# Optimization experiments

Hardware: AMD Instinct MI355X
Metric: run time of the kernel (lower is better)

The kernel has to match this reference:

```python
import jax, jax.numpy as jnp
import numpy as np
jax.config.update("jax_enable_x64", True)

B, S, E, H, L, FF = 2, 1024, 768, 12, 4, 2048
MAX_THOUGHT_LEN = 3
LN_EPS = 1e-5

def _sinusoidal_pe(max_len, d):
    pos = np.arange(max_len)[:, None]
    div = np.exp(np.arange(0, d, 2) * (-np.log(10000.0) / d))
    pe = np.zeros((max_len, d), np.float32)
    pe[:, 0::2] = np.sin(pos * div)
    pe[:, 1::2] = np.cos(pos * div)
    return jnp.asarray(pe)

def _build_mask(Smax, thoughts_taken, n_tokens):
    # Vectorized equivalent of the torch loop building the block-causal mask.
    bs = thoughts_taken + 1
    i = np.arange(Smax)[:, None]
    j = np.arange(Smax)[None, :]
    same_block = (i // bs == j // bs) & (i // bs < n_tokens) & ((i % bs) >= (j % bs))
    start_vis = ((j % bs) == 0) & (j // bs < n_tokens) & (i > j) & (i < n_tokens * bs)
    allowed = same_block | start_vis
    # TransformerEncoder canonicalizes the bool mask: True (disallowed) -> -inf additive
    return jnp.asarray(np.where(allowed, 0.0, -np.inf).astype(np.float64))

def _layernorm(x, w, b):
    mu = jnp.mean(x, -1, keepdims=True)
    var = jnp.mean((x - mu) ** 2, -1, keepdims=True)
    return (x - mu) / jnp.sqrt(var + LN_EPS) * w + b

def setup_inputs() -> dict:
    key = jax.random.key(0)
    ks = jax.random.split(key, 8)
    f32 = jnp.float32
    return {
        "x": jax.random.normal(ks[0], (B, S, E), f32),
        "padding_mask": jnp.zeros((B, S), bool),
        "thought_pe": jax.random.normal(ks[1], (MAX_THOUGHT_LEN + 1, E), f32),
        "Wqkv": jax.random.normal(ks[2], (L, 3 * E, E), f32) * (E ** -0.5),
        "bqkv": jnp.zeros((L, 3 * E), f32),
        "W1": jax.random.normal(ks[3], (L, FF, E), f32) * (E ** -0.5),
        "b1": jnp.zeros((L, FF), f32),
        "W2": jax.random.normal(ks[4], (L, E, FF), f32) * (FF ** -0.5),
        "b2": jnp.zeros((L, E), f32),
        "ln1_w": jnp.ones((L, E), f32), "ln1_b": jnp.zeros((L, E), f32),
        "ln2_w": jnp.ones((L, E), f32), "ln2_b": jnp.zeros((L, E), f32),
        "lnf_w": jnp.ones((E,), f32), "lnf_b": jnp.zeros((E,), f32),
        "thoughts_taken": 1,
        "real_token_count": 512,
    }

def reference(x, padding_mask, thought_pe, Wqkv, bqkv, W1, b1, W2, b2,
              ln1_w, ln1_b, ln2_w, ln2_b, lnf_w, lnf_b,
              thoughts_taken, real_token_count):
    # NOTE: padding_mask is accepted but unused, matching the custom layer.
    nt = thoughts_taken + 1
    pe = _sinusoidal_pe(S, E)
    # DualPositionalEncoding (eval mode -> dropout is identity)
    h = x[:, : real_token_count * nt].reshape(B, real_token_count, nt, E)
    h = h + pe[:real_token_count][None, :, None, :] + thought_pe[:nt][None, None, :, :]
    h = h.reshape(B, real_token_count * nt, E)
    pad = S - real_token_count * nt
    if pad > 0:
        h = jnp.pad(h, ((0, 0), (0, pad), (0, 0)))
    mask = _build_mask(S, thoughts_taken, real_token_count)
    scale = 1.0 / jnp.sqrt(jnp.float64(E // H))
    for l in range(L):
        # manual fp64 attention, exactly as the torch layer
        s64 = h.astype(jnp.float64)
        qkv = s64 @ Wqkv[l].astype(jnp.float64).T + bqkv[l].astype(jnp.float64)
        q, k, v = jnp.split(qkv, 3, axis=-1)
        rh = lambda t: t.reshape(B, S, H, E // H).transpose(0, 2, 1, 3)
        q, k, v = rh(q), rh(k), rh(v)
        scores = jnp.einsum("bhqd,bhkd->bhqk", q, k) * scale + mask
        attn = jax.nn.softmax(scores, axis=-1)
        ao = jnp.einsum("bhqk,bhkd->bhqd", attn, v).transpose(0, 2, 1, 3).reshape(B, S, E)
        # NOTE: no out_proj -- the custom forward skips self_attn.out_proj
        h = _layernorm(h + ao.astype(h.dtype), ln1_w[l], ln1_b[l])
        ff = jax.nn.gelu(h @ W1[l].T + b1[l], approximate=False) @ W2[l].T + b2[l]
        h = _layernorm(h + ff, ln2_w[l], ln2_b[l])
        h = jnp.nan_to_num(h)
    return _layernorm(h, lnf_w, lnf_b)
```

## Files before the change

kernel.cpp:

```cpp
#include <hip/hip_runtime.h>
#include <math.h>

#define SEQ 1024
#define EMB 768
#define NHEAD 12
#define HDIM 64
#define NLAYER 4
#define FFDIM 2048
#define BATCH 2
#define ROWS (BATCH * SEQ)
#define BH (BATCH * NHEAD)
#define NCHUNK 2
#define CTILES 8

using f16 = _Float16;
using f16x4 = __attribute__((ext_vector_type(4))) _Float16;
using f16x8 = __attribute__((ext_vector_type(8))) _Float16;
using f32x4 = __attribute__((ext_vector_type(4))) float;
using f32x16 = __attribute__((ext_vector_type(16))) float;
typedef unsigned long long u64;

__device__ inline void gload16(const void* g, void* l) {
    __builtin_amdgcn_global_load_lds((const __attribute__((address_space(1))) unsigned*)g,
                                     (__attribute__((address_space(3))) unsigned*)l, 16, 0, 0);
}

__global__ void prep_kernel(const float* __restrict__ Wq, int na,
                            const float* __restrict__ W1, int nb,
                            const float* __restrict__ W2, int nc,
                            f16* __restrict__ oq, f16* __restrict__ o1, f16* __restrict__ o2,
                            const float* __restrict__ x,
                            const float* __restrict__ tpe,
                            float* __restrict__ h32,
                            f16* __restrict__ h16,
                            u64* __restrict__ mtab,
                            const int* __restrict__ tt_p,
                            const int* __restrict__ rtc_p) {
    const int ncast = na + nb + nc;
    const int nembed = BATCH * SEQ * EMB;
    const int nmask = SEQ * 16;
    const int total = ncast + nembed + nmask;
    const int nt = *tt_p + 1;
    const int rtc = *rtc_p;
    for (int i = blockIdx.x * blockDim.x + threadIdx.x; i < total;
         i += gridDim.x * blockDim.x) {
        if (i < ncast) {
            const float* src;
            f16* dst;
            int off;
            if (i < na)            { src = Wq; dst = oq; off = i; }
            else if (i < na + nb)  { src = W1; dst = o1; off = i - na; }
            else                   { src = W2; dst = o2; off = i - na - nb; }
            float4 v = ((const float4*)src)[off];
            f16x4 o;
            o[0] = (f16)v.x; o[1] = (f16)v.y; o[2] = (f16)v.z; o[3] = (f16)v.w;
            ((f16x4*)dst)[off] = o;
        } else if (i < ncast + nembed) {
            int idx = i - ncast;
            int e = idx % EMB;
            int s = (idx / EMB) % SEQ;
            float val;
            if (s < rtc * nt) {
                int p = s / nt;
                int t = s % nt;
                int i2 = e & ~1;
                float div = __expf((float)i2 * -0.0119926314f);
                float ang = (float)p * div;
                float pe = (e & 1) ? __cosf(ang) : __sinf(ang);
                val = x[idx] + pe + tpe[t * EMB + e];
            } else {
                val = 0.0f;
            }
            h32[idx] = val;
            h16[idx] = (f16)val;
        } else {
            int idx = i - ncast - nembed;
            int ii = idx >> 4, jt = idx & 15;
            int id = ii / nt, im = ii % nt;
            int iok = (ii < rtc * nt);
            u64 m = 0;
            for (int k = 0; k < 64; k++) {
                int j = jt * 64 + k;
                int jd = j / nt, jm = j % nt;
                bool same = (id == jd) && (id < rtc) && (im >= jm);
                bool sv   = (jm == 0) && (jd < rtc) && (ii > j) && iok;
                if (same || sv) m |= (1ull << k);
            }
            mtab[idx] = m;
        }
    }
}

template<int ACT, int OUT>
__global__ __launch_bounds__(512) void gemm_f16(const f16* __restrict__ A,
                                                const f16* __restrict__ W,
                                                const float* __restrict__ bias,
                                                f16* __restrict__ Ch,
                                                f16* __restrict__ vtg,
                                                int M, int N, int K) {
    __shared__ f16 As[2][128 * 64];
    __shared__ f16 Ws[2][128 * 64];
    const int tid = threadIdx.x, lane = tid & 63, wave = tid >> 6;
    const int gx = gridDim.x;
    const int nwg = gx * gridDim.y;
    int orig = blockIdx.y * gx + blockIdx.x;
    int nid = (nwg & 7) ? orig : ((orig & 7) * (nwg >> 3) + (orig >> 3));
    const int bm = (nid / gx) * 128, bn = (nid % gx) * 128;
    const int l31 = lane & 31, l32 = lane >> 5;
    const int wm = (wave >> 1) * 32, wn = (wave & 1) * 64;
    const int srow = lane >> 3, sslot = lane & 7;
    const int klen = K / gridDim.z;
    const int kbeg = blockIdx.z * klen;
    const int nsteps = klen >> 6;

    f32x16 acc[2];
#pragma unroll
    for (int ni = 0; ni < 2; ni++)
#pragma unroll
        for (int e = 0; e < 16; e++) acc[ni][e] = 0.f;

#pragma unroll
    for (int i = 0; i < 2; i++) {
        int R0 = wave * 16 + i * 8;
        int row = R0 + srow;
        int gs = (sslot ^ (row & 7)) << 3;
        gload16(A + (size_t)(bm + row) * K + kbeg + gs, As[0] + R0 * 64);
        gload16(W + (size_t)(bn + row) * K + kbeg + gs, Ws[0] + R0 * 64);
    }
    __syncthreads();

    int cur = 0;
    for (int t = 0; t < nsteps; t++) {
        if (t + 1 < nsteps) {
            int k1 = kbeg + (t + 1) * 64;
            int nxt = cur ^ 1;
#pragma unroll
            for (int i = 0; i < 2; i++) {
                int R0 = wave * 16 + i * 8;
                int row = R0 + srow;
                int gs = (sslot ^ (row & 7)) << 3;
                gload16(A + (size_t)(bm + row) * K + k1 + gs, As[nxt] + R0 * 64);
                gload16(W + (size_t)(bn + row) * K + k1 + gs, Ws[nxt] + R0 * 64);
            }
        }
#pragma unroll
        for (int ks = 0; ks < 4; ks++) {
            int kslot = ks * 2 + l32;
            f16x8 a, b[2];
            {
                int row = wm + l31;
                a = *(const f16x8*)(As[cur] + row * 64 + ((kslot ^ (row & 7)) << 3));
            }
#pragma unroll
            for (int ni = 0; ni < 2; ni++) {
                int row = wn + ni * 32 + l31;
                b[ni] = *(const f16x8*)(Ws[cur] + row * 64 + ((kslot ^ (row & 7)) << 3));
            }
#pragma unroll
            for (int ni = 0; ni < 2; ni++)
                acc[ni] = __builtin_amdgcn_mfma_f32_32x32x16_f16(a, b[ni], acc[ni], 0, 0, 0);
        }
        __syncthreads();
        cur ^= 1;
    }

#pragma unroll
    for (int ni = 0; ni < 2; ni++) {
        int nbase = bn + wn + ni * 32;
        int n = nbase + l31;
        if (OUT == 3) {
            f16* dst = Ch + (size_t)blockIdx.z * ROWS * N;
#pragma unroll
            for (int reg = 0; reg < 16; reg++) {
                int m = bm + wm + (reg & 3) + 8 * (reg >> 2) + 4 * l32;
                dst[(size_t)m * N + n] = (f16)acc[ni][reg];
            }
        } else {
            float bv = bias[n];
            if (OUT != 2 || nbase < 2 * EMB) {
                int cstride = (OUT == 2) ? 2 * EMB : N;
#pragma unroll
                for (int reg = 0; reg < 16; reg++) {
                    int m = bm + wm + (reg & 3) + 8 * (reg >> 2) + 4 * l32;
                    float v = acc[ni][reg] + bv;
                    if (ACT) v = 0.5f * v * (1.0f + erff(v * 0.70710678118654752f));
                    Ch[(size_t)m * cstride + n] = (f16)v;
                }
            } else {
                int d = n - 2 * EMB;
                int hh = d >> 6, dd = d & 63;
#pragma unroll
                for (int q = 0; q < 4; q++) {
                    int m0 = bm + wm + 8 * q + 4 * l32;
                    int bb = m0 >> 10, s0 = m0 & (SEQ - 1);
                    f16x4 pack;
#pragma unroll
                    for (int r = 0; r < 4; r++) pack[r] = (f16)(acc[ni][4 * q + r] + bv);
                    *(f16x4*)(vtg + ((size_t)((bb * NHEAD + hh) * HDIM + dd)) * SEQ + s0) = pack;
                }
            }
        }
    }
}

__global__ __launch_bounds__(256) void attn_part(const f16* __restrict__ qk,
                                                 const f16* __restrict__ vtg,
                                                 const u64* __restrict__ mtab,
                                                 f16* __restrict__ po,
                                                 float* __restrict__ pm,
                                                 float* __restrict__ pl) {
    const int c = blockIdx.x;
    const int qt = blockIdx.y;
    if (c * CTILES > qt) return;
    const int bh = blockIdx.z;
    const int b = bh / NHEAD, hh = bh % NHEAD;
    const int q0 = qt * 64;
    const int jt_beg = c * CTILES, jt_end = min(qt, c * CTILES + CTILES - 1);

    __shared__ f16 Qs[64 * 64];
    __shared__ f16 Ks[2][64 * 64];
    __shared__ f16 VT[2][64 * 64];
    __shared__ f16 Ps[4 * 16 * 64];

    const int tid = threadIdx.x, lane = tid & 63, wave = tid >> 6;
    const int l15 = lane & 15, l16 = lane >> 4;
    const int RS = 2 * EMB;
    const f16* vth = vtg + (size_t)(b * NHEAD + hh) * HDIM * SEQ;
    const float SCALE2 = 0.125f * 1.44269504088896f;

#pragma unroll
    for (int it = 0; it < 2; it++) {
        int R0 = wave * 16 + it * 8;
        int row = R0 + (lane >> 3), slot = lane & 7;
        int gs = (slot ^ (row & 7)) << 3;
        gload16(qk + (size_t)(b * SEQ + q0 + row) * RS + hh * HDIM + gs, Qs + R0 * 64);
        gload16(qk + (size_t)(b * SEQ + jt_beg * 64 + row) * RS + EMB + hh * HDIM + gs,
                Ks[0] + R0 * 64);
        gload16(vth + (size_t)row * SEQ + jt_beg * 64 + gs, VT[0] + R0 * 64);
    }
    __syncthreads();

    f16x8 qa[2];
#pragma unroll
    for (int ks = 0; ks < 2; ks++) {
        int row = wave * 16 + l15;
        int kslot = l16 + ks * 4;
        qa[ks] = *(const f16x8*)(Qs + row * 64 + ((kslot ^ (row & 7)) << 3));
    }

    float mrow[4], lsum[4];
    f32x4 o[4];
    int iglob[4];
#pragma unroll
    for (int r = 0; r < 4; r++) {
        mrow[r] = -1e30f; lsum[r] = 0.f;
        iglob[r] = q0 + wave * 16 + l16 * 4 + r;
    }
#pragma unroll
    for (int nf = 0; nf < 4; nf++) o[nf] = (f32x4){0.f, 0.f, 0.f, 0.f};

    for (int jt = jt_beg; jt <= jt_end; jt++) {
        const int cur = (jt - jt_beg) & 1;
        if (jt < jt_end) {
            const int nxt = cur ^ 1;
            const int jn0 = (jt + 1) * 64;
#pragma unroll
            for (int it = 0; it < 2; it++) {
                int R0 = wave * 16 + it * 8;
                int row = R0 + (lane >> 3), slot = lane & 7;
                int gs = (slot ^ (row & 7)) << 3;
                gload16(qk + (size_t)(b * SEQ + jn0 + row) * RS + EMB + hh * HDIM + gs,
                        Ks[nxt] + R0 * 64);
                gload16(vth + (size_t)row * SEQ + jn0 + gs, VT[nxt] + R0 * 64);
            }
        }

        unsigned mlo[4], mhi[4];
#pragma unroll
        for (int r = 0; r < 4; r++) {
            u64 mk = mtab[iglob[r] * 16 + jt];
            mlo[r] = (unsigned)mk;
            mhi[r] = (unsigned)(mk >> 32);
        }

        f32x4 s[4];
        __builtin_amdgcn_s_setprio(1);
#pragma unroll
        for (int nf = 0; nf < 4; nf++) {
            s[nf] = (f32x4){0.f, 0.f, 0.f, 0.f};
#pragma unroll
            for (int ks = 0; ks < 2; ks++) {
                int row = nf * 16 + l15;
                int kslot = l16 + ks * 4;
                f16x8 kb = *(const f16x8*)(Ks[cur] + row * 64 + ((kslot ^ (row & 7)) << 3));
                s[nf] = __builtin_amdgcn_mfma_f32_16x16x32_f16(qa[ks], kb, s[nf], 0, 0, 0);
            }
        }
        __builtin_amdgcn_s_setprio(0);

        float p[4][4];
        float tmax[4] = {-1e30f, -1e30f, -1e30f, -1e30f};
#pragma unroll
        for (int nf = 0; nf < 4; nf++) {
            int sh = (nf & 1) * 16 + l15;
#pragma unroll
            for (int r = 0; r < 4; r++) {
                unsigned w = (nf & 2) ? mhi[r] : mlo[r];
                bool allowed = (w >> sh) & 1;
                float val = allowed ? s[nf][r] * SCALE2 : -1e30f;
                p[nf][r] = val;
                tmax[r] = fmaxf(tmax[r], val);
            }
        }
#pragma unroll
        for (int r = 0; r < 4; r++) {
            tmax[r] = fmaxf(tmax[r], __shfl_xor(tmax[r], 1));
            tmax[r] = fmaxf(tmax[r], __shfl_xor(tmax[r], 2));
            tmax[r] = fmaxf(tmax[r], __shfl_xor(tmax[r], 4));
            tmax[r] = fmaxf(tmax[r], __shfl_xor(tmax[r], 8));
        }
        float alpha[4], rsum[4], meff[4];
#pragma unroll
        for (int r = 0; r < 4; r++) {
            float mn = fmaxf(mrow[r], tmax[r]);
            alpha[r] = exp2f(mrow[r] - mn);
            mrow[r] = mn;
            meff[r] = (mn <= -1e29f) ? 0.f : mn;
            rsum[r] = 0.f;
        }
#pragma unroll
        for (int nf = 0; nf < 4; nf++)
#pragma unroll
            for (int r = 0; r < 4; r++) {
                float e = exp2f(p[nf][r] - meff[r]);
                p[nf][r] = e;
                rsum[r] += e;
            }
#pragma unroll
        for (int r = 0; r < 4; r++) {
            rsum[r] += __shfl_xor(rsum[r], 1);
            rsum[r] += __shfl_xor(rsum[r], 2);
            rsum[r] += __shfl_xor(rsum[r], 4);
            rsum[r] += __shfl_xor(rsum[r], 8);
            lsum[r] = lsum[r] * alpha[r] + rsum[r];
        }
#pragma unroll
        for (int nf = 0; nf < 4; nf++)
#pragma unroll
            for (int r = 0; r < 4; r++) o[nf][r] *= alpha[r];

        f16* P = Ps + wave * 16 * 64;
#pragma unroll
        for (int nf = 0; nf < 4; nf++)
#pragma unroll
            for (int r = 0; r < 4; r++) {
                int prow = l16 * 4 + r;
                int pcol = nf * 16 + l15;
                P[prow * 64 + (((pcol >> 3) ^ (prow & 7)) << 3) + (pcol & 7)] = (f16)p[nf][r];
            }

        __builtin_amdgcn_s_setprio(1);
#pragma unroll
        for (int ks = 0; ks < 2; ks++) {
            int kslot = l16 + ks * 4;
            int prow = l15;
            f16x8 pa = *(const f16x8*)(P + prow * 64 + ((kslot ^ (prow & 7)) << 3));
#pragma unroll
            for (int nf = 0; nf < 4; nf++) {
                int vrow = nf * 16 + l15;
                f16x8 vb = *(const f16x8*)(VT[cur] + vrow * 64 + ((kslot ^ (vrow & 7)) << 3));
                o[nf] = __builtin_amdgcn_mfma_f32_16x16x32_f16(pa, vb, o[nf], 0, 0, 0);
            }
        }
        __builtin_amdgcn_s_setprio(0);
        __syncthreads();
    }

    const size_t base = (size_t)(c * BH + bh) * SEQ;
#pragma unroll
    for (int r = 0; r < 4; r++) {
        int i = q0 + wave * 16 + l16 * 4 + r;
#pragma unroll
        for (int nf = 0; nf < 4; nf++)
            po[(base + i) * 64 + nf * 16 + l15] = (f16)o[nf][r];
        if (l15 == 0) {
            pm[base + i] = mrow[r];
            pl[base + i] = lsum[r];
        }
    }
}

__global__ __launch_bounds__(256) void add_ln_attn(const float* __restrict__ X,
                                                   const f16* __restrict__ po,
                                                   const float* __restrict__ pm,
                                                   const float* __restrict__ pl,
                                                   const float* __restrict__ w,
                                                   const float* __restrict__ bsh,
                                                   float* __restrict__ out32,
                                                   f16* __restrict__ out16) {
    const int row = blockIdx.x * 4 + (threadIdx.x >> 6);
    const int lane = threadIdx.x & 63;
    const int b = row >> 10, i = row & (SEQ - 1);
    const int nch = (i >> 6) / CTILES + 1;
    const float* xr = X + (size_t)row * EMB;
    float4 v[3];
    float s = 0.f;
#pragma unroll
    for (int t = 0; t < 3; t++) {
        int e = t * 256 + lane * 4;
        int hh = e >> 6, d = e & 63;
        size_t hbase = (size_t)(b * NHEAD + hh) * SEQ + i;
        float m = -1e30f;
        for (int c = 0; c < nch; c++) m = fmaxf(m, pm[hbase + (size_t)c * BH * SEQ]);
        float meff = (m <= -1e29f) ? 0.f : m;
        float lt = 0.f;
        float4 ov = {0.f, 0.f, 0.f, 0.f};
        for (int c = 0; c < nch; c++) {
            size_t idx = hbase + (size_t)c * BH * SEQ;
            float wgt = exp2f(pm[idx] - meff);
            lt += pl[idx] * wgt;
            f16x4 pv = *(const f16x4*)(po + idx * 64 + d);
            ov.x += (float)pv[0] * wgt; ov.y += (float)pv[1] * wgt;
            ov.z += (float)pv[2] * wgt; ov.w += (float)pv[3] * wgt;
        }
        float inv = (lt > 0.f) ? 1.0f / lt : 0.0f;
        float4 a = *(const float4*)(xr + e);
        a.x += ov.x * inv; a.y += ov.y * inv; a.z += ov.z * inv; a.w += ov.w * inv;
        v[t] = a;
        s += a.x + a.y + a.z + a.w;
    }
#pragma unroll
    for (int k = 1; k < 64; k <<= 1) s += __shfl_xor(s, k);
    float mu = s * (1.0f / EMB);
    float s2 = 0.f;
#pragma unroll
    for (int t = 0; t < 3; t++) {
        float dx = v[t].x - mu, dy = v[t].y - mu, dz = v[t].z - mu, dw = v[t].w - mu;
        s2 += dx * dx + dy * dy + dz * dz + dw * dw;
    }
#pragma unroll
    for (int k = 1; k < 64; k <<= 1) s2 += __shfl_xor(s2, k);
    float inv = rsqrtf(s2 * (1.0f / EMB) + 1e-5f);
#pragma unroll
    for (int t = 0; t < 3; t++) {
        int e = t * 256 + lane * 4;
        float4 wv = *(const float4*)(w + e);
        float4 bv = *(const float4*)(bsh + e);
        float4 o;
        o.x = (v[t].x - mu) * inv * wv.x + bv.x;
        o.y = (v[t].y - mu) * inv * wv.y + bv.y;
        o.z = (v[t].z - mu) * inv * wv.z + bv.z;
        o.w = (v[t].w - mu) * inv * wv.w + bv.w;
        *(float4*)(out32 + (size_t)row * EMB + e) = o;
        f16x4 hh;
        hh[0] = (f16)o.x; hh[1] = (f16)o.y; hh[2] = (f16)o.z; hh[3] = (f16)o.w;
        *(f16x4*)(out16 + (size_t)row * EMB + e) = hh;
    }
}

template<int FINAL>
__global__ __launch_bounds__(256) void add_ln_split4(const float* __restrict__ X,
                                                     const f16* __restrict__ part,
                                                     const float* __restrict__ bias,
                                                     const float* __restrict__ w,
                                                     const float* __restrict__ bsh,
                                                     const float* __restrict__ wf,
                                                     const float* __restrict__ bf,
                                                     float* __restrict__ out32,
                                                     f16* __restrict__ out16) {
    const int row = blockIdx.x * 4 + (threadIdx.x >> 6);
    const int lane = threadIdx.x & 63;
    const float* xr = X + (size_t)row * EMB;
    float4 v[3];
    float s = 0.f;
#pragma unroll
    for (int t = 0; t < 3; t++) {
        int e = t * 256 + lane * 4;
        float4 a = *(const float4*)(xr + e);
        float4 bb = *(const float4*)(bias + e);
        a.x += bb.x; a.y += bb.y; a.z += bb.z; a.w += bb.w;
#pragma unroll
        for (int z = 0; z < 4; z++) {
            f16x4 pz = *(const f16x4*)(part + (size_t)z * ROWS * EMB + (size_t)row * EMB + e);
            a.x += (float)pz[0]; a.y += (float)pz[1];
            a.z += (float)pz[2]; a.w += (float)pz[3];
        }
        v[t] = a;
        s += a.x + a.y + a.z + a.w;
    }
#pragma unroll
    for (int k = 1; k < 64; k <<= 1) s += __shfl_xor(s, k);
    float mu = s * (1.0f / EMB);
    float s2 = 0.f;
#pragma unroll
    for (int t = 0; t < 3; t++) {
        float dx = v[t].x - mu, dy = v[t].y - mu, dz = v[t].z - mu, dw = v[t].w - mu;
        s2 += dx * dx + dy * dy + dz * dz + dw * dw;
    }
#pragma unroll
    for (int k = 1; k < 64; k <<= 1) s2 += __shfl_xor(s2, k);
    float inv = rsqrtf(s2 * (1.0f / EMB) + 1e-5f);
    float4 o2[3];
    float sF = 0.f;
#pragma unroll
    for (int t = 0; t < 3; t++) {
        int e = t * 256 + lane * 4;
        float4 wv = *(const float4*)(w + e);
        float4 bv = *(const float4*)(bsh + e);
        float4 o;
        o.x = (v[t].x - mu) * inv * wv.x + bv.x;
        o.y = (v[t].y - mu) * inv * wv.y + bv.y;
        o.z = (v[t].z - mu) * inv * wv.z + bv.z;
        o.w = (v[t].w - mu) * inv * wv.w + bv.w;
        o2[t] = o;
        if (FINAL) sF += o.x + o.y + o.z + o.w;
        else {
            *(float4*)(out32 + (size_t)row * EMB + e) = o;
            f16x4 hh;
            hh[0] = (f16)o.x; hh[1] = (f16)o.y; hh[2] = (f16)o.z; hh[3] = (f16)o.w;
            *(f16x4*)(out16 + (size_t)row * EMB + e) = hh;
        }
    }
    if (FINAL) {
#pragma unroll
        for (int k = 1; k < 64; k <<= 1) sF += __shfl_xor(sF, k);
        float muF = sF * (1.0f / EMB);
        float s2F = 0.f;
#pragma unroll
        for (int t = 0; t < 3; t++) {
            float dx = o2[t].x - muF, dy = o2[t].y - muF, dz = o2[t].z - muF, dw = o2[t].w - muF;
            s2F += dx * dx + dy * dy + dz * dz + dw * dw;
        }
#pragma unroll
        for (int k = 1; k < 64; k <<= 1) s2F += __shfl_xor(s2F, k);
        float invF = rsqrtf(s2F * (1.0f / EMB) + 1e-5f);
#pragma unroll
        for (int t = 0; t < 3; t++) {
            int e = t * 256 + lane * 4;
            float4 wv = *(const float4*)(wf + e);
            float4 bv = *(const float4*)(bf + e);
            float4 o;
            o.x = (o2[t].x - muF) * invF * wv.x + bv.x;
            o.y = (o2[t].y - muF) * invF * wv.y + bv.y;
            o.z = (o2[t].z - muF) * invF * wv.z + bv.z;
            o.w = (o2[t].w - muF) * invF * wv.w + bv.w;
            *(float4*)(out32 + (size_t)row * EMB + e) = o;
        }
    }
}

extern "C" void kernel_launch(void* const* d_in, const int* in_sizes, int n_in,
                              void* d_out, int out_size, void* d_ws, size_t ws_size,
                              hipStream_t stream) {
    const float* x      = (const float*)d_in[0];
    const float* tpe    = (const float*)d_in[2];
    const float* Wqkv   = (const float*)d_in[3];
    const float* bqkv   = (const float*)d_in[4];
    const float* W1     = (const float*)d_in[5];
    const float* b1     = (const float*)d_in[6];
    const float* W2     = (const float*)d_in[7];
    const float* b2     = (const float*)d_in[8];
    const float* ln1_w  = (const float*)d_in[9];
    const float* ln1_b  = (const float*)d_in[10];
    const float* ln2_w  = (const float*)d_in[11];
    const float* ln2_b  = (const float*)d_in[12];
    const float* lnf_w  = (const float*)d_in[13];
    const float* lnf_b  = (const float*)d_in[14];
    const int*   tt     = (const int*)d_in[15];
    const int*   rtc    = (const int*)d_in[16];
    float* out = (float*)d_out;

    char* wsp = (char*)d_ws;
    float* h32  = (float*)wsp;
    f16*   h16  = (f16*)(wsp + 6291456);
    f16*   act  = (f16*)(wsp + 9437184);
    f16*   vtg  = (f16*)(wsp + 17825792);
    f16*   part = (f16*)(wsp + 20971520);
    f16*   wbuf = (f16*)(wsp + 33554432);
    f16*   po   = (f16*)(wsp + 72876032);
    float* pm   = (float*)(wsp + 79167488);
    float* pl   = (float*)(wsp + 79364096);
    u64*   mtab = (u64*)(wsp + 79560704);

    const int EQ = 3 * EMB * EMB;
    const int E1 = FFDIM * EMB;
    const int E2 = EMB * FFDIM;
    f16* wqAll = wbuf;
    f16* w1All = wbuf + (size_t)NLAYER * EQ;
    f16* w2All = w1All + (size_t)NLAYER * E1;

    prep_kernel<<<4096, 256, 0, stream>>>(Wqkv, NLAYER * EQ / 4, W1, NLAYER * E1 / 4,
                                          W2, NLAYER * E2 / 4, wqAll, w1All, w2All,
                                          x, tpe, h32, h16, mtab, tt, rtc);

    for (int l = 0; l < NLAYER; l++) {
        const f16* wq16 = wqAll + (size_t)l * EQ;
        const f16* w116 = w1All + (size_t)l * E1;
        const f16* w216 = w2All + (size_t)l * E2;
        const float* bq  = bqkv + (size_t)l * 3 * EMB;
        const float* bb1 = b1 + (size_t)l * FFDIM;
        const float* bb2 = b2 + (size_t)l * EMB;

        gemm_f16<0, 2><<<dim3(3 * EMB / 128, ROWS / 128), 512, 0, stream>>>(
            h16, wq16, bq, act, vtg, ROWS, 3 * EMB, EMB);

        attn_part<<<dim3(NCHUNK, SEQ / 64, BH), 256, 0, stream>>>(act, vtg, mtab, po, pm, pl);

        add_ln_attn<<<ROWS / 4, 256, 0, stream>>>(h32, po, pm, pl,
                                                  ln1_w + l * EMB, ln1_b + l * EMB, h32, h16);

        gemm_f16<1, 1><<<dim3(FFDIM / 128, ROWS / 128), 512, 0, stream>>>(
            h16, w116, bb1, act, nullptr, ROWS, FFDIM, EMB);

        gemm_f16<0, 3><<<dim3(EMB / 128, ROWS / 128, 4), 512, 0, stream>>>(
            act, w216, nullptr, part, nullptr, ROWS, EMB, FFDIM);

        if (l < NLAYER - 1)
            add_ln_split4<0><<<ROWS / 4, 256, 0, stream>>>(h32, part, bb2,
                ln2_w + l * EMB, ln2_b + l * EMB, nullptr, nullptr, h32, h16);
        else
            add_ln_split4<1><<<ROWS / 4, 256, 0, stream>>>(h32, part, bb2,
                ln2_w + l * EMB, ln2_b + l * EMB, lnf_w, lnf_b, out, nullptr);
    }
}
```

Before: 396.7 us.

## Triple-buffer GEMM LDS tiles with explicit vmcnt waits and wave priority

Moves the f16 GEMM from a double-buffered LDS pipeline to a triple-buffered one. Each iteration keeps two tiles of global-to-LDS loads in flight, waits with a partial s_waitcnt vmcnt, and uses a single raw barrier per step. It also raises wave priority around the MFMA block. The aim is to hide global load latency better, at the cost of 1.5x the LDS per workgroup (96KB), which may lower occupancy. The raw barrier also relies on the vmcnt accounting being exact.

New measurement: 463.0 us. 1.17x slower.

```diff
diff --git a/kernel.cpp b/kernel.cpp
--- a/kernel.cpp
+++ b/kernel.cpp
@@ -98,8 +98,8 @@
                                                 f16* __restrict__ Ch,
                                                 f16* __restrict__ vtg,
                                                 int M, int N, int K) {
-    __shared__ f16 As[2][128 * 64];
-    __shared__ f16 Ws[2][128 * 64];
+    __shared__ f16 As[3][128 * 64];
+    __shared__ f16 Ws[3][128 * 64];
     const int tid = threadIdx.x, lane = tid & 63, wave = tid >> 6;
     const int gx = gridDim.x;
     const int nwg = gx * gridDim.y;
@@ -119,30 +119,34 @@
 #pragma unroll
         for (int e = 0; e < 16; e++) acc[ni][e] = 0.f;
 
-#pragma unroll
-    for (int i = 0; i < 2; i++) {
-        int R0 = wave * 16 + i * 8;
-        int row = R0 + srow;
-        int gs = (sslot ^ (row & 7)) << 3;
-        gload16(A + (size_t)(bm + row) * K + kbeg + gs, As[0] + R0 * 64);
-        gload16(W + (size_t)(bn + row) * K + kbeg + gs, Ws[0] + R0 * 64);
-    }
-    __syncthreads();
-
-    int cur = 0;
+    const int R0a = wave * 16, R0b = wave * 16 + 8;
+    const int rowa = R0a + srow, rowb = R0b + srow;
+    const int gsa = (sslot ^ (rowa & 7)) << 3;
+    const int gsb = (sslot ^ (rowb & 7)) << 3;
+
+#define STAGE(buf, k0)                                                          \
+    do {                                                                        \
+        gload16(A + (size_t)(bm + rowa) * K + (k0) + gsa, As[buf] + R0a * 64);  \
+        gload16(A + (size_t)(bm + rowb) * K + (k0) + gsb, As[buf] + R0b * 64);  \
+        gload16(W + (size_t)(bn + rowa) * K + (k0) + gsa, Ws[buf] + R0a * 64);  \
+        gload16(W + (size_t)(bn + rowb) * K + (k0) + gsb, Ws[buf] + R0b * 64);  \
+    } while (0)
+
+    STAGE(0, kbeg);
+    STAGE(1, kbeg + 64);
+
     for (int t = 0; t < nsteps; t++) {
-        if (t + 1 < nsteps) {
-            int k1 = kbeg + (t + 1) * 64;
-            int nxt = cur ^ 1;
-#pragma unroll
-            for (int i = 0; i < 2; i++) {
-                int R0 = wave * 16 + i * 8;
-                int row = R0 + srow;
-                int gs = (sslot ^ (row & 7)) << 3;
-                gload16(A + (size_t)(bm + row) * K + k1 + gs, As[nxt] + R0 * 64);
-                gload16(W + (size_t)(bn + row) * K + k1 + gs, Ws[nxt] + R0 * 64);
-            }
-        }
+        const int cur = t % 3;
+        if (t < nsteps - 1) {
+            asm volatile("s_waitcnt vmcnt(4)" ::: "memory");
+        } else {
+            asm volatile("s_waitcnt vmcnt(0)" ::: "memory");
+        }
+        __builtin_amdgcn_s_barrier();
+        if (t + 2 < nsteps) {
+            STAGE((t + 2) % 3, kbeg + (t + 2) * 64);
+        }
+        __builtin_amdgcn_s_setprio(1);
 #pragma unroll
         for (int ks = 0; ks < 4; ks++) {
             int kslot = ks * 2 + l32;
@@ -160,9 +164,9 @@
             for (int ni = 0; ni < 2; ni++)
                 acc[ni] = __builtin_amdgcn_mfma_f32_32x32x16_f16(a, b[ni], acc[ni], 0, 0, 0);
         }
-        __syncthreads();
-        cur ^= 1;
-    }
+        __builtin_amdgcn_s_setprio(0);
+    }
+#undef STAGE
 
 #pragma unroll
     for (int ni = 0; ni < 2; ni++) {
```
